# Kernel tuning notes

Hardware: AMD Instinct MI355X
Metric: run time of the kernel (lower is better)

The kernel has to match this reference:

```python
import jax, jax.numpy as jnp
import numpy as np

L, C, B = 256, 20, 1024


def _pos_mask(L):
    # pairwise mask: l2 - l1 >= 1, shape (L, L); broadcast over channels
    ls = jnp.arange(L)
    return (ls[None, :] - ls[:, None]) >= 1


def setup_inputs() -> dict:
    key = jax.random.key(0)
    k0, k1, k2 = jax.random.split(key, 3)
    x_lc = jax.random.uniform(k0, (B, L, C), dtype=jnp.float32)
    theta_0 = jnp.zeros((1,), dtype=jnp.float32)
    theta_lc = jax.random.normal(k1, (1, L, C), dtype=jnp.float32) / np.sqrt(L)
    pm = _pos_mask(L)
    theta_lclc = (jax.random.normal(k2, (1, L, C, L, C), dtype=jnp.float32)
                  / np.sqrt(L * L)) * pm[None, :, None, :, None]
    mask = pm
    return {"x_lc": x_lc, "theta_0": theta_0, "theta_lc": theta_lc,
            "theta_lclc": theta_lclc, "mask": mask}


def reference(x_lc, theta_0, theta_lc, theta_lclc, mask):
    Bn = x_lc.shape[0]
    # additive term: sum_{l,c} theta_lc * x
    phi = theta_0 + jnp.einsum('blc,zlc->b', x_lc, theta_lc)[:, None]
    # pairwise term as a masked bilinear form: x^T (mask * theta) x
    # (avoids materializing the (B,L,C,L,C) broadcast of the original)
    theta_m = theta_lclc[0] * mask[:, None, :, None].astype(theta_lclc.dtype)
    LC = L * C
    xf = x_lc.reshape(Bn, LC)                      # (B, LC)
    tf_ = theta_m.reshape(LC, LC)                  # (LC, LC)
    pair = jnp.einsum('bi,ij,bj->b', xf, tf_, xf)  # two GEMMs under the hood
    phi = phi + pair[:, None]
    return phi
```

## Files before the change

kernel.cpp:

```cpp
#include <hip/hip_runtime.h>
#include <stdint.h>

#define LDIM 256
#define CDIM 20
#define LC   5120
#define NB   1024
#define BM   128
#define BN   256
#define NSEG 40
#define ITOT 3280

typedef __attribute__((ext_vector_type(8))) short short8;
typedef __attribute__((ext_vector_type(4))) float float4v;
typedef __attribute__((ext_vector_type(4))) unsigned int uint4v;
typedef unsigned short ushort_t;

#define TB_BYTES (52428800ull)
#define XB_BYTES (10485760ull)
#define WS_NEED  (TB_BYTES + XB_BYTES)

__device__ inline uint32_t pack_bf16x2(float a, float b) {
    uint32_t ua = __float_as_uint(a);
    uint32_t ub = __float_as_uint(b);
    ua += 0x7fffu + ((ua >> 16) & 1u);
    ub += 0x7fffu + ((ub >> 16) & 1u);
    return (ua >> 16) | (ub & 0xffff0000u);
}

__device__ inline void load_lds16(const void* g, void* l) {
    __builtin_amdgcn_global_load_lds(
        (const __attribute__((address_space(1))) uint32_t*)g,
        (__attribute__((address_space(3))) uint32_t*)l, 16, 0, 0);
}

__device__ inline int swz(int r) { return (r ^ (r >> 2)) & 3; }

__global__ __launch_bounds__(256) void conv_kernel(
    const float* __restrict__ T, const float* __restrict__ X,
    const float* __restrict__ th0, const float* __restrict__ thlc,
    ushort_t* __restrict__ Tb, ushort_t* __restrict__ Xb,
    float* __restrict__ out)
{
    const int bid = blockIdx.x;
    const int t   = threadIdx.x;
    __shared__ float red[4];

    if (bid < LC) {
        const int r  = bid;
        const int tk = (r >> 7) << 7;
        const float*  src = T  + (size_t)r * LC;
        ushort_t*     dst = Tb + (size_t)r * LC;
        for (int c = tk + t * 4; c < LC; c += 1024) {
            float4 f = *(const float4*)(src + c);
            uint2 u;
            u.x = pack_bf16x2(f.x, f.y);
            u.y = pack_bf16x2(f.z, f.w);
            *(uint2*)(dst + c) = u;
        }
    } else {
        const int b = bid - LC;
        const float*  src = X  + (size_t)b * LC;
        ushort_t*     dst = Xb + (size_t)b * LC;
        float s = 0.f;
        for (int c = t * 4; c < LC; c += 1024) {
            float4 f = *(const float4*)(src + c);
            float4 w = *(const float4*)(thlc + c);
            s += f.x * w.x + f.y * w.y + f.z * w.z + f.w * w.w;
            uint2 u;
            u.x = pack_bf16x2(f.x, f.y);
            u.y = pack_bf16x2(f.z, f.w);
            *(uint2*)(dst + c) = u;
        }
        s += __shfl_xor(s, 1);  s += __shfl_xor(s, 2);  s += __shfl_xor(s, 4);
        s += __shfl_xor(s, 8);  s += __shfl_xor(s, 16); s += __shfl_xor(s, 32);
        if ((t & 63) == 0) red[t >> 6] = s;
        __syncthreads();
        if (t == 0) out[b] = th0[0] + red[0] + red[1] + red[2] + red[3];
    }
}

__global__ __launch_bounds__(256, 2) void pair_bf(
    const ushort_t* __restrict__ Tb, const ushort_t* __restrict__ Xb,
    const float* __restrict__ X, float* __restrict__ out)
{
    const int n    = blockIdx.x;
    const int bcol = n & 3;
    const int kblk = n >> 2;
    const int bn0  = bcol * BN;

    const int gbeg = (ITOT * kblk) >> 7;
    const int gend = (ITOT * (kblk + 1)) >> 7;

    int it = 0, pre = 0;
    while (pre + (160 - (it << 2)) <= gbeg) { pre += 160 - (it << 2); ++it; }
    const int li = gbeg - pre;

    __shared__ __align__(16) ushort_t A_s[2][512 * 8];
    __shared__ __align__(16) ushort_t B_s[2][1024 * 8];

    const int t    = threadIdx.x;
    const int lane = t & 63;
    const int wid  = t >> 6;
    const int wm   = (wid >> 1) * 64;
    const int wn   = (wid & 1) * 128;
    const int l16  = lane & 15;
    const int qk   = lane >> 4;

    int rowA[2], offA[2];
    #pragma unroll
    for (int j = 0; j < 2; ++j) {
        const int c = (wid << 7) + (j << 6) + lane;
        rowA[j] = c >> 2;
        offA[j] = (((c & 3) ^ swz(rowA[j])) << 3);
    }
    int rowB[4], offB[4];
    #pragma unroll
    for (int j = 0; j < 4; ++j) {
        const int c = (wid << 8) + (j << 6) + lane;
        rowB[j] = c >> 2;
        offB[j] = (((c & 3) ^ swz(rowB[j])) << 3);
    }

    int adrA[4], adrB[8];
    #pragma unroll
    for (int mt = 0; mt < 4; ++mt) {
        const int r = wm + mt * 16 + l16;
        adrA[mt] = (r * 4 + (qk ^ swz(r))) * 16;
    }
    #pragma unroll
    for (int nt = 0; nt < 8; ++nt) {
        const int r = wn + nt * 16 + l16;
        adrB[nt] = (r * 4 + (qk ^ swz(r))) * 16;
    }

    const ushort_t* gA[2];
    const ushort_t* gB[4];
    int itI = it, liI = li, nI = 160 - (it << 2);

    auto rebaseI = [&]() {
        const int kc = (itI << 7) + (liI << 5);
        #pragma unroll
        for (int j = 0; j < 2; ++j)
            gA[j] = Tb + (size_t)((itI << 7) + rowA[j]) * LC + kc + offA[j];
        #pragma unroll
        for (int j = 0; j < 4; ++j)
            gB[j] = Xb + (size_t)(bn0 + rowB[j]) * LC + kc + offB[j];
    };
    auto issue = [&](int cb) {
        #pragma unroll
        for (int j = 0; j < 2; ++j) {
            load_lds16(gA[j], &A_s[cb][((wid << 7) + (j << 6)) * 8]);
            gA[j] += 32;
        }
        #pragma unroll
        for (int j = 0; j < 4; ++j) {
            load_lds16(gB[j], &B_s[cb][((wid << 8) + (j << 6)) * 8]);
            gB[j] += 32;
        }
    };
    auto advI = [&]() {
        ++liI;
        if (liI == nI) {
            ++itI; liI = 0;
            if (itI < NSEG) { nI = 160 - (itI << 2); rebaseI(); }
        }
    };

    float4v acc[4][8];
    #pragma unroll
    for (int mt = 0; mt < 4; ++mt)
        #pragma unroll
        for (int nt = 0; nt < 8; ++nt)
            #pragma unroll
            for (int r = 0; r < 4; ++r) acc[mt][nt][r] = 0.f;

    int itC = it, liC = li, nC = nI;

    rebaseI();
    issue(0);
    advI();

    int cur = 0;
    for (int g = gbeg; g < gend; ++g) {
        __syncthreads();
        if (g + 1 < gend) { issue(cur ^ 1); advI(); }

        {
            const ushort_t* As = A_s[cur];
            const ushort_t* Bs = B_s[cur];
            short8 af[4], bfr[8];
            #pragma unroll
            for (int mt = 0; mt < 4; ++mt)
                af[mt] = *(const short8*)((const char*)As + adrA[mt]);
            #pragma unroll
            for (int nt = 0; nt < 8; ++nt)
                bfr[nt] = *(const short8*)((const char*)Bs + adrB[nt]);
            #pragma unroll
            for (int mt = 0; mt < 4; ++mt)
                #pragma unroll
                for (int nt = 0; nt < 8; ++nt)
                    acc[mt][nt] = __builtin_amdgcn_mfma_f32_16x16x32_bf16(
                        af[mt], bfr[nt], acc[mt][nt], 0, 0, 0);
        }

        ++liC;
        if (liC == nC || g + 1 == gend) {
            const int i0 = itC << 7;
            #pragma unroll
            for (int nt = 0; nt < 8; ++nt) {
                const int b = bn0 + wn + nt * 16 + l16;
                const float* xb = X + (size_t)b * LC + i0 + wm + qk * 4;
                float s = 0.f;
                #pragma unroll
                for (int mt = 0; mt < 4; ++mt) {
                    float4 xv = *(const float4*)(xb + mt * 16);
                    s += acc[mt][nt][0] * xv.x + acc[mt][nt][1] * xv.y +
                         acc[mt][nt][2] * xv.z + acc[mt][nt][3] * xv.w;
                }
                s += __shfl_xor(s, 16);
                s += __shfl_xor(s, 32);
                if (qk == 0) atomicAdd(&out[b], s);
            }
            #pragma unroll
            for (int mt = 0; mt < 4; ++mt)
                #pragma unroll
                for (int nt = 0; nt < 8; ++nt)
                    #pragma unroll
                    for (int r = 0; r < 4; ++r) acc[mt][nt][r] = 0.f;
            ++itC; liC = 0; nC = 160 - (itC << 2);
        }
        cur ^= 1;
    }
}

__global__ __launch_bounds__(256) void init_kernel(
    const float* __restrict__ x, const float* __restrict__ th0,
    const float* __restrict__ thlc, float* __restrict__ out)
{
    const int b = blockIdx.x;
    const float4* xb = (const float4*)(x + (size_t)b * LC);
    const float4* tv = (const float4*)thlc;
    float s = 0.f;
    for (int i = threadIdx.x; i < LC / 4; i += 256) {
        float4 a = xb[i], t = tv[i];
        s += a.x * t.x + a.y * t.y + a.z * t.z + a.w * t.w;
    }
    s += __shfl_xor(s, 1);  s += __shfl_xor(s, 2);  s += __shfl_xor(s, 4);
    s += __shfl_xor(s, 8);  s += __shfl_xor(s, 16); s += __shfl_xor(s, 32);
    __shared__ float red[4];
    if ((threadIdx.x & 63) == 0) red[threadIdx.x >> 6] = s;
    __syncthreads();
    if (threadIdx.x == 0) out[b] = th0[0] + red[0] + red[1] + red[2] + red[3];
}

__global__ __launch_bounds__(256) void pair_kernel(
    const float* __restrict__ T, const float* __restrict__ X,
    float* __restrict__ out)
{
    const int n  = blockIdx.x;
    const int r  = n & 7;
    const int g  = n >> 3;
    const int i0  = (g >> 3) * BM;
    const int bn0 = (g & 7) * 128;
    const int kstart = i0;
    const int nIter  = (LC - kstart) >> 6;
    const int ipc    = (nIter + 7) >> 3;
    const int itBeg  = r * ipc;
    const int itEnd  = (itBeg + ipc < nIter) ? (itBeg + ipc) : nIter;
    if (itBeg >= itEnd) return;
    const int kbeg   = kstart + (itBeg << 6);

    __shared__ __align__(16) short A_s[8 * BM * 8];
    __shared__ __align__(16) short B_s[8 * BM * 8];

    const int t    = threadIdx.x;
    const int lane = t & 63;
    const int wid  = t >> 6;
    const int wm   = (wid >> 1) * 64;
    const int wn   = (wid & 1) * 64;
    const int l16  = lane & 15;
    const int qk   = lane >> 4;

    const float* pA[4]; const float* pB[4]; int sIdx[4];
    #pragma unroll
    for (int u = 0; u < 4; ++u) {
        const int id  = t + u * 256;
        const int row = id >> 3;
        const int kq  = id & 7;
        pA[u] = T + (size_t)(i0 + row) * LC + kbeg + kq * 8;
        pB[u] = X + (size_t)(bn0 + row) * LC + kbeg + kq * 8;
        sIdx[u] = (kq * BM + (row ^ kq)) * 8;
    }

    float4v acc[4][4] = {};
    for (int itr = itBeg; itr < itEnd; ++itr) {
        __syncthreads();
        #pragma unroll
        for (int u = 0; u < 4; ++u) {
            float4 a0 = ((const float4*)pA[u])[0];
            float4 a1 = ((const float4*)pA[u])[1];
            float4 b0 = ((const float4*)pB[u])[0];
            float4 b1 = ((const float4*)pB[u])[1];
            pA[u] += 64; pB[u] += 64;
            uint4v va, vb;
            va[0] = pack_bf16x2(a0.x, a0.y); va[1] = pack_bf16x2(a0.z, a0.w);
            va[2] = pack_bf16x2(a1.x, a1.y); va[3] = pack_bf16x2(a1.z, a1.w);
            vb[0] = pack_bf16x2(b0.x, b0.y); vb[1] = pack_bf16x2(b0.z, b0.w);
            vb[2] = pack_bf16x2(b1.x, b1.y); vb[3] = pack_bf16x2(b1.z, b1.w);
            *(uint4v*)(A_s + sIdx[u]) = va;
            *(uint4v*)(B_s + sIdx[u]) = vb;
        }
        __syncthreads();
        #pragma unroll
        for (int step = 0; step < 2; ++step) {
            const int kf = step * 4 + qk;
            short8 af[4], bfr[4];
            #pragma unroll
            for (int mt = 0; mt < 4; ++mt)
                af[mt] = *(const short8*)(A_s + (kf * BM + ((wm + mt * 16 + l16) ^ kf)) * 8);
            #pragma unroll
            for (int nt = 0; nt < 4; ++nt)
                bfr[nt] = *(const short8*)(B_s + (kf * BM + ((wn + nt * 16 + l16) ^ kf)) * 8);
            #pragma unroll
            for (int mt = 0; mt < 4; ++mt)
                #pragma unroll
                for (int nt = 0; nt < 4; ++nt)
                    acc[mt][nt] = __builtin_amdgcn_mfma_f32_16x16x32_bf16(
                        af[mt], bfr[nt], acc[mt][nt], 0, 0, 0);
        }
    }
    #pragma unroll
    for (int nt = 0; nt < 4; ++nt) {
        const int b = bn0 + wn + nt * 16 + l16;
        const float* xb = X + (size_t)b * LC + i0 + wm + qk * 4;
        float s = 0.f;
        #pragma unroll
        for (int mt = 0; mt < 4; ++mt) {
            float4 xv = *(const float4*)(xb + mt * 16);
            s += acc[mt][nt][0] * xv.x + acc[mt][nt][1] * xv.y +
                 acc[mt][nt][2] * xv.z + acc[mt][nt][3] * xv.w;
        }
        s += __shfl_xor(s, 16);
        s += __shfl_xor(s, 32);
        if (qk == 0) atomicAdd(&out[b], s);
    }
}

extern "C" void kernel_launch(void* const* d_in, const int* in_sizes, int n_in,
                              void* d_out, int out_size, void* d_ws, size_t ws_size,
                              hipStream_t stream) {
    const float* x    = (const float*)d_in[0];
    const float* th0  = (const float*)d_in[1];
    const float* thlc = (const float*)d_in[2];
    const float* T    = (const float*)d_in[3];
    float* out = (float*)d_out;

    if (ws_size >= WS_NEED) {
        ushort_t* Tb = (ushort_t*)d_ws;
        ushort_t* Xb = (ushort_t*)((char*)d_ws + TB_BYTES);
        conv_kernel<<<LC + NB, 256, 0, stream>>>(T, x, th0, thlc, Tb, Xb, out);
        pair_bf<<<512, 256, 0, stream>>>(Tb, Xb, x, out);
    } else {
        init_kernel<<<NB, 256, 0, stream>>>(x, th0, thlc, out);
        pair_kernel<<<(LC / BM) * (NB / 128) * 8, 256, 0, stream>>>(T, x, out);
    }
}
```

Baseline: 224.1 us.

## Use 64-wide K tiles with single-buffered LDS, remapped blocks, bf16 epilogue X

The GEMM K-step in the pair kernel grows from 32 to 64 with an 8-way XOR swizzle, and LDS double buffering is dropped in favor of a load, sync, compute pattern with two MFMA sub-steps per tile. Block indices are remapped so neighboring blocks share B columns and K ranges, which should improve L2 locality. The epilogue now reads the bf16 copy of X instead of fp32 X, cutting bytes read. Losing the prefetch overlap means global load latency is exposed each iteration, and the bf16 epilogue X adds some rounding error.

Result: faster. 211.9 us (-5.4%).

```diff
diff --git a/kernel.cpp b/kernel.cpp
--- a/kernel.cpp
+++ b/kernel.cpp
@@ -7,8 +7,7 @@
 #define NB   1024
 #define BM   128
 #define BN   256
-#define NSEG 40
-#define ITOT 3280
+#define ITOT64 1640
 
 typedef __attribute__((ext_vector_type(8))) short short8;
 typedef __attribute__((ext_vector_type(4))) float float4v;
@@ -27,13 +26,15 @@
     return (ua >> 16) | (ub & 0xffff0000u);
 }
 
+__device__ inline float bf16_to_f32(ushort_t u) {
+    return __uint_as_float(((uint32_t)u) << 16);
+}
+
 __device__ inline void load_lds16(const void* g, void* l) {
     __builtin_amdgcn_global_load_lds(
         (const __attribute__((address_space(1))) uint32_t*)g,
         (__attribute__((address_space(3))) uint32_t*)l, 16, 0, 0);
 }
-
-__device__ inline int swz(int r) { return (r ^ (r >> 2)) & 3; }
 
 __global__ __launch_bounds__(256) void conv_kernel(
     const float* __restrict__ T, const float* __restrict__ X,
@@ -81,22 +82,21 @@
 
 __global__ __launch_bounds__(256, 2) void pair_bf(
     const ushort_t* __restrict__ Tb, const ushort_t* __restrict__ Xb,
-    const float* __restrict__ X, float* __restrict__ out)
+    float* __restrict__ out)
 {
     const int n    = blockIdx.x;
-    const int bcol = n & 3;
-    const int kblk = n >> 2;
-    const int bn0  = bcol * BN;
-
-    const int gbeg = (ITOT * kblk) >> 7;
-    const int gend = (ITOT * (kblk + 1)) >> 7;
+    const int kblk = (n & 7) | (((n >> 5) & 15) << 3);
+    const int bn0  = ((n >> 3) & 3) * BN;
+
+    const int gbeg = (ITOT64 * kblk) >> 7;
+    const int gend = (ITOT64 * (kblk + 1)) >> 7;
 
     int it = 0, pre = 0;
-    while (pre + (160 - (it << 2)) <= gbeg) { pre += 160 - (it << 2); ++it; }
-    const int li = gbeg - pre;
-
-    __shared__ __align__(16) ushort_t A_s[2][512 * 8];
-    __shared__ __align__(16) ushort_t B_s[2][1024 * 8];
+    while (pre + (80 - 2 * it) <= gbeg) { pre += 80 - 2 * it; ++it; }
+    int li = gbeg - pre;
+
+    __shared__ __align__(16) ushort_t A_s[1024 * 8];
+    __shared__ __align__(16) ushort_t B_s[2048 * 8];
 
     const int t    = threadIdx.x;
     const int lane = t & 63;
@@ -106,95 +106,70 @@
     const int l16  = lane & 15;
     const int qk   = lane >> 4;
 
-    int rowA[2], offA[2];
-    #pragma unroll
-    for (int j = 0; j < 2; ++j) {
-        const int c = (wid << 7) + (j << 6) + lane;
-        rowA[j] = c >> 2;
-        offA[j] = (((c & 3) ^ swz(rowA[j])) << 3);
-    }
-    int rowB[4], offB[4];
+    uint32_t offA[4];
     #pragma unroll
     for (int j = 0; j < 4; ++j) {
         const int c = (wid << 8) + (j << 6) + lane;
-        rowB[j] = c >> 2;
-        offB[j] = (((c & 3) ^ swz(rowB[j])) << 3);
-    }
-
-    int adrA[4], adrB[8];
-    #pragma unroll
-    for (int mt = 0; mt < 4; ++mt) {
-        const int r = wm + mt * 16 + l16;
-        adrA[mt] = (r * 4 + (qk ^ swz(r))) * 16;
-    }
-    #pragma unroll
-    for (int nt = 0; nt < 8; ++nt) {
-        const int r = wn + nt * 16 + l16;
-        adrB[nt] = (r * 4 + (qk ^ swz(r))) * 16;
-    }
-
-    const ushort_t* gA[2];
-    const ushort_t* gB[4];
-    int itI = it, liI = li, nI = 160 - (it << 2);
-
-    auto rebaseI = [&]() {
-        const int kc = (itI << 7) + (liI << 5);
-        #pragma unroll
-        for (int j = 0; j < 2; ++j)
-            gA[j] = Tb + (size_t)((itI << 7) + rowA[j]) * LC + kc + offA[j];
+        const int row = c >> 3;
+        const int g = (c & 7) ^ (row & 7);
+        offA[j] = (uint32_t)row * LC + (g << 3);
+    }
+    uint32_t offB[8];
+    #pragma unroll
+    for (int j = 0; j < 8; ++j) {
+        const int c = (wid << 9) + (j << 6) + lane;
+        const int row = c >> 3;
+        const int g = (c & 7) ^ (row & 7);
+        offB[j] = (uint32_t)(bn0 + row) * LC + (g << 3);
+    }
+
+    int adrA[2][4], adrB[2][8];
+    #pragma unroll
+    for (int step = 0; step < 2; ++step) {
+        const int kf = step * 4 + qk;
+        #pragma unroll
+        for (int mt = 0; mt < 4; ++mt) {
+            const int r = wm + mt * 16 + l16;
+            adrA[step][mt] = ((r << 3) + (kf ^ (r & 7))) << 4;
+        }
+        #pragma unroll
+        for (int nt = 0; nt < 8; ++nt) {
+            const int r = wn + nt * 16 + l16;
+            adrB[step][nt] = ((r << 3) + (kf ^ (r & 7))) << 4;
+        }
+    }
+
+    int   i0    = it << 7;
+    int   k0    = i0 + (li << 6);
+    size_t baseA = (size_t)i0 * LC + k0;
+
+    float4v acc[4][8];
+    #pragma unroll
+    for (int mt = 0; mt < 4; ++mt)
+        #pragma unroll
+        for (int nt = 0; nt < 8; ++nt)
+            #pragma unroll
+            for (int r = 0; r < 4; ++r) acc[mt][nt][r] = 0.f;
+
+    for (int g = gbeg; g < gend; ++g) {
+        __syncthreads();
         #pragma unroll
         for (int j = 0; j < 4; ++j)
-            gB[j] = Xb + (size_t)(bn0 + rowB[j]) * LC + kc + offB[j];
-    };
-    auto issue = [&](int cb) {
-        #pragma unroll
-        for (int j = 0; j < 2; ++j) {
-            load_lds16(gA[j], &A_s[cb][((wid << 7) + (j << 6)) * 8]);
-            gA[j] += 32;
-        }
-        #pragma unroll
-        for (int j = 0; j < 4; ++j) {
-            load_lds16(gB[j], &B_s[cb][((wid << 8) + (j << 6)) * 8]);
-            gB[j] += 32;
-        }
-    };
-    auto advI = [&]() {
-        ++liI;
-        if (liI == nI) {
-            ++itI; liI = 0;
-            if (itI < NSEG) { nI = 160 - (itI << 2); rebaseI(); }
-        }
-    };
-
-    float4v acc[4][8];
-    #pragma unroll
-    for (int mt = 0; mt < 4; ++mt)
-        #pragma unroll
-        for (int nt = 0; nt < 8; ++nt)
-            #pragma unroll
-            for (int r = 0; r < 4; ++r) acc[mt][nt][r] = 0.f;
-
-    int itC = it, liC = li, nC = nI;
-
-    rebaseI();
-    issue(0);
-    advI();
-
-    int cur = 0;
-    for (int g = gbeg; g < gend; ++g) {
-        __syncthreads();
-        if (g + 1 < gend) { issue(cur ^ 1); advI(); }
-
-        {
-            const ushort_t* As = A_s[cur];
-            const ushort_t* Bs = B_s[cur];
+            load_lds16(Tb + baseA + offA[j], A_s + (((wid << 8) + (j << 6)) << 3));
+        #pragma unroll
+        for (int j = 0; j < 8; ++j)
+            load_lds16(Xb + k0 + offB[j],   B_s + (((wid << 9) + (j << 6)) << 3));
+        __syncthreads();
+
+        #pragma unroll
+        for (int step = 0; step < 2; ++step) {
             short8 af[4], bfr[8];
             #pragma unroll
             for (int mt = 0; mt < 4; ++mt)
-                af[mt] = *(const short8*)((const char*)As + adrA[mt]);
+                af[mt] = *(const short8*)((const char*)A_s + adrA[step][mt]);
             #pragma unroll
             for (int nt = 0; nt < 8; ++nt)
-                bfr[nt] = *(const short8*)((const char*)Bs + adrB[nt]);
+                bfr[nt] = *(const short8*)((const char*)B_s + adrB[step][nt]);
             #pragma unroll
             for (int mt = 0; mt < 4; ++mt)
                 #pragma unroll
@@ -203,19 +178,21 @@
                         af[mt], bfr[nt], acc[mt][nt], 0, 0, 0);
         }
 
-        ++liC;
-        if (liC == nC || g + 1 == gend) {
-            const int i0 = itC << 7;
+        ++li;
+        const bool segEnd = (li == 80 - 2 * it);
+        if (segEnd || g + 1 == gend) {
             #pragma unroll
             for (int nt = 0; nt < 8; ++nt) {
                 const int b = bn0 + wn + nt * 16 + l16;
-                const float* xb = X + (size_t)b * LC + i0 + wm + qk * 4;
+                const ushort_t* xb = Xb + (size_t)b * LC + i0 + wm + qk * 4;
                 float s = 0.f;
                 #pragma unroll
                 for (int mt = 0; mt < 4; ++mt) {
-                    float4 xv = *(const float4*)(xb + mt * 16);
-                    s += acc[mt][nt][0] * xv.x + acc[mt][nt][1] * xv.y +
-                         acc[mt][nt][2] * xv.z + acc[mt][nt][3] * xv.w;
+                    ushort4 xv = *(const ushort4*)(xb + mt * 16);
+                    s += acc[mt][nt][0] * bf16_to_f32(xv.x)
+                       + acc[mt][nt][1] * bf16_to_f32(xv.y)
+                       + acc[mt][nt][2] * bf16_to_f32(xv.z)
+                       + acc[mt][nt][3] * bf16_to_f32(xv.w);
                 }
                 s += __shfl_xor(s, 16);
                 s += __shfl_xor(s, 32);
@@ -227,9 +204,18 @@
                 for (int nt = 0; nt < 8; ++nt)
                     #pragma unroll
                     for (int r = 0; r < 4; ++r) acc[mt][nt][r] = 0.f;
-            ++itC; liC = 0; nC = 160 - (itC << 2);
-        }
-        cur ^= 1;
+        }
+        if (segEnd) {
+            ++it; li = 0;
+            if (it < 40) {
+                i0 = it << 7;
+                k0 = i0;
+                baseA = (size_t)i0 * LC + k0;
+            }
+        } else {
+            k0 += 64;
+            baseA += 64;
+        }
     }
 }
 
@@ -359,7 +345,7 @@
         ushort_t* Tb = (ushort_t*)d_ws;
         ushort_t* Xb = (ushort_t*)((char*)d_ws + TB_BYTES);
         conv_kernel<<<LC + NB, 256, 0, stream>>>(T, x, th0, thlc, Tb, Xb, out);
-        pair_bf<<<512, 256, 0, stream>>>(Tb, Xb, x, out);
+        pair_bf<<<512, 256, 0, stream>>>(Tb, Xb, out);
     } else {
         init_kernel<<<NB, 256, 0, stream>>>(x, th0, thlc, out);
         pair_kernel<<<(LC / BM) * (NB / 128) * 8, 256, 0, stream>>>(T, x, out);
```
